# Performance work log

Measured on AMD Instinct MI355X. Metric: run time of the kernel, lower is better.

## Reference

```python
import jax, jax.numpy as jnp
import numpy as np

# Bahdanau additive attention (eval mode: dropout is identity):
#   fac1 = W @ k        [B, d, S]
#   fac2 = U @ q        [B, d, S]
#   s    = v^T tanh(fac1 + fac2)   [B, 1, S]
#   attn = softmax(s, axis=-1)

B, D, S = 32, 1024, 2048


def setup_inputs() -> dict:
    key = jax.random.key(0)
    kq, kk, kv, kW, kU = jax.random.split(key, 5)
    scale = 1.0 / np.sqrt(D)
    return {
        "q": jax.random.normal(kq, (B, D, S), dtype=jnp.float32),
        "k": jax.random.normal(kk, (B, D, S), dtype=jnp.float32),
        "v": jax.random.normal(kv, (B, D, 1), dtype=jnp.float32),
        "W": jax.random.normal(kW, (D, D), dtype=jnp.float32) * scale,
        "U": jax.random.normal(kU, (D, D), dtype=jnp.float32) * scale,
    }


def reference(q, k, v, W, U):
    # projections: [d,e] x [b,e,s] -> [b,d,s]
    fac1 = jnp.einsum("de,bes->bds", W, k)
    fac2 = jnp.einsum("de,bes->bds", U, q)
    e = jnp.tanh(fac1 + fac2)            # [B, D, S]
    s = jnp.einsum("bdo,bds->bos", v, e)  # [B, 1, S]
    attn = jax.nn.softmax(s, axis=-1)     # softmax over sequence
    return attn
```

## Files before the change

kernel.cpp:

```cpp
#include <hip/hip_runtime.h>

#define D_ 1024
#define S_ 2048
#define B_ 32
#define BM 256
#define BN 256
#define BK 64
#define NKT 32
#define NPH 64

typedef __attribute__((ext_vector_type(8))) _Float16 f16x8;
typedef __attribute__((ext_vector_type(16))) float f32x16;

__device__ __forceinline__ void async_ld16(const void* g, void* l) {
  __builtin_amdgcn_global_load_lds(
      (const __attribute__((address_space(1))) void*)g,
      (__attribute__((address_space(3))) void*)l, 16, 0, 0);
}

__global__ void prep_kernel(const float* __restrict__ W, const float* __restrict__ U,
                            _Float16* __restrict__ wf, _Float16* __restrict__ uf) {
  int t = blockIdx.x * blockDim.x + threadIdx.x;
  const float* src = blockIdx.y ? U : W;
  _Float16* dst = blockIdx.y ? uf : wf;

  int tile = t >> 11;
  int g    = t & 2047;
  int top  = g >> 6;
  int ks = top >> 3, wr = (top >> 2) & 1, fm = top & 3;
  int lane = g & 63, l31 = lane & 31, lhi = lane >> 5;
  int row   = wr * 128 + fm * 32 + l31;
  int chunk = ks * 2 + lhi;
  int d = (tile >> 4) * 256 + row;
  int e = (tile & 15) * 64 + chunk * 8;

  const float* p = src + (size_t)d * D_ + e;
  f16x8 hv;
#pragma unroll
  for (int j = 0; j < 8; ++j) hv[j] = (_Float16)p[j];
  *(f16x8*)(dst + (size_t)t * 8) = hv;
}

__global__ void kqprep_kernel(const float* __restrict__ kten, const float* __restrict__ qten,
                              _Float16* __restrict__ bfmt) {
  size_t t = (size_t)blockIdx.x * 256 + threadIdx.x;
  int g    = (int)(t & 2047);
  int tile = (int)(t >> 11);
  int st   = tile & 7;
  int ktt  = (tile >> 3) & 15;
  int half = (tile >> 7) & 1;
  int b    = tile >> 8;
  int l31 = g & 31, clh = (g >> 5) & 1, w2 = (g >> 6) & 7, cks = g >> 9;
  int n = w2 * 32 + l31;
  int c = cks * 2 + clh;
  int e = ktt * 64 + c * 8;
  int s = st * 256 + n;

  const float* src = (half ? qten : kten) + (size_t)b * (D_ * S_) + (size_t)e * S_ + s;
  f16x8 hv;
#pragma unroll
  for (int j = 0; j < 8; ++j) hv[j] = (_Float16)src[(size_t)j * S_];
  *(f16x8*)(bfmt + t * 8) = hv;
}

__global__ void __launch_bounds__(512, 2)
gemm_kernel(const float* __restrict__ v,
            const _Float16* __restrict__ wf, const _Float16* __restrict__ uf,
            const _Float16* __restrict__ bfmt,
            float* __restrict__ partials) {
  __shared__ __align__(16) _Float16 Af[4][BM * 32];
  __shared__ __align__(16) _Float16 Bf[4][BN * 32];
  __shared__ float vbuf[BM];
  __shared__ float red[2][BN];

  const int tid  = threadIdx.x;
  const int lane = tid & 63;
  const int wid  = tid >> 6;
  const int wr   = wid >> 2;
  const int wc   = wid & 3;

  int bid  = blockIdx.x;
  int g    = ((bid >> 5) << 3) | (bid & 7);
  int dblk = (bid >> 3) & 3;
  int st   = g & 7;
  int b    = g >> 3;
  int s0   = st * BN;

  if (tid < BM) vbuf[tid] = v[(size_t)b * D_ + dblk * BM + tid];
  __syncthreads();

  f32x16 acc[4][2];
#pragma unroll
  for (int i = 0; i < 4; ++i)
#pragma unroll
    for (int j = 0; j < 2; ++j)
#pragma unroll
      for (int r = 0; r < 16; ++r) acc[i][j][r] = 0.0f;

#define PH_FENCE asm volatile("" ::: "memory")
#define WAIT8 asm volatile("s_waitcnt vmcnt(8)" ::: "memory")
#define WAIT4 asm volatile("s_waitcnt vmcnt(4)" ::: "memory")
#define WAIT0 asm volatile("s_waitcnt vmcnt(0)" ::: "memory")

#define GLLH(h_) do {                                                          \
    const int kt_ = (h_) >> 1, hh_ = (h_) & 1, bi_ = (h_) & 3;                 \
    const int half_ = kt_ >> 4, ktt_ = kt_ & 15;                               \
    const _Float16* at_ = (half_ ? uf : wf)                                    \
        + (size_t)(dblk * 16 + ktt_) * 16384 + (size_t)hh_ * 8192;             \
    const _Float16* bt_ = bfmt                                                 \
        + ((size_t)(((b * 2 + half_) * 16 + ktt_) * 8 + st)) * 16384           \
        + (size_t)hh_ * 8192;                                                  \
    async_ld16(at_ + (size_t)tid * 8,         &Af[bi_][(size_t)tid * 8]);      \
    async_ld16(at_ + (size_t)(tid + 512) * 8, &Af[bi_][(size_t)(tid + 512) * 8]); \
    async_ld16(bt_ + (size_t)tid * 8,         &Bf[bi_][(size_t)tid * 8]);      \
    async_ld16(bt_ + (size_t)(tid + 512) * 8, &Bf[bi_][(size_t)(tid + 512) * 8]); \
  } while (0)

#define PHASE(h_, ISSUE, WAITC) do {                                           \
    PH_FENCE;                                                                  \
    const int bi_ = (h_) & 3;                                                  \
    f16x8 a0_[4], a1_[4], b0_[2], b1_[2];                                      \
    _Pragma("unroll")                                                          \
    for (int fm = 0; fm < 4; ++fm)                                             \
      a0_[fm] = *(const f16x8*)&Af[bi_][(size_t)(((wr * 4 + fm) * 64 + lane)) * 8]; \
    _Pragma("unroll")                                                          \
    for (int fn = 0; fn < 2; ++fn)                                             \
      b0_[fn] = *(const f16x8*)&Bf[bi_][(size_t)(((wc * 2 + fn) * 64 + lane)) * 8]; \
    _Pragma("unroll")                                                          \
    for (int fm = 0; fm < 4; ++fm)                                             \
      a1_[fm] = *(const f16x8*)&Af[bi_][(size_t)(((8 + wr * 4 + fm) * 64 + lane)) * 8]; \
    _Pragma("unroll")                                                          \
    for (int fn = 0; fn < 2; ++fn)                                             \
      b1_[fn] = *(const f16x8*)&Bf[bi_][(size_t)(((8 + wc * 2 + fn) * 64 + lane)) * 8]; \
    ISSUE;                                                                     \
    __builtin_amdgcn_s_barrier();                                              \
    __builtin_amdgcn_s_setprio(1);                                             \
    _Pragma("unroll")                                                          \
    for (int fm = 0; fm < 4; ++fm)                                             \
      _Pragma("unroll")                                                        \
      for (int fn = 0; fn < 2; ++fn)                                           \
        acc[fm][fn] = __builtin_amdgcn_mfma_f32_32x32x16_f16(a0_[fm], b0_[fn], acc[fm][fn], 0, 0, 0); \
    _Pragma("unroll")                                                          \
    for (int fm = 0; fm < 4; ++fm)                                             \
      _Pragma("unroll")                                                        \
      for (int fn = 0; fn < 2; ++fn)                                           \
        acc[fm][fn] = __builtin_amdgcn_mfma_f32_32x32x16_f16(a1_[fm], b1_[fn], acc[fm][fn], 0, 0, 0); \
    __builtin_amdgcn_s_setprio(0);                                             \
    WAITC;                                                                     \
    __builtin_amdgcn_s_barrier();                                              \
    __builtin_amdgcn_sched_barrier(0);                                         \
  } while (0)

  PH_FENCE;
  GLLH(0); GLLH(1); GLLH(2);
  WAIT8;
  __builtin_amdgcn_s_barrier();
  __builtin_amdgcn_sched_barrier(0);

  for (int h = 0; h < NPH - 3; ++h) {
    PHASE(h, GLLH(h + 3), WAIT8);
  }
  PHASE(61, , WAIT4);
  PHASE(62, , WAIT0);
  PHASE(63, , );

#undef PHASE
#undef GLLH
#undef WAIT0
#undef WAIT4
#undef WAIT8
#undef PH_FENCE

  float psum[2] = {0.f, 0.f};
#pragma unroll
  for (int fm = 0; fm < 4; ++fm)
#pragma unroll
    for (int fn = 0; fn < 2; ++fn)
#pragma unroll
      for (int r = 0; r < 16; ++r) {
        int row = wr * 128 + fm * 32 + (r & 3) + 8 * (r >> 2) + 4 * (lane >> 5);
        float x  = acc[fm][fn][r];
        float th = 1.0f - 2.0f / (__expf(2.0f * x) + 1.0f);
        psum[fn] += vbuf[row] * th;
      }
#pragma unroll
  for (int fn = 0; fn < 2; ++fn) psum[fn] += __shfl_xor(psum[fn], 32);
  if (lane < 32) {
    red[wr][wc * 64 + lane]      = psum[0];
    red[wr][wc * 64 + 32 + lane] = psum[1];
  }
  __syncthreads();
  if (tid < BN) {
    float val = red[0][tid] + red[1][tid];
    partials[(size_t)(dblk * B_ + b) * S_ + s0 + tid] = val;
  }
}

__global__ void __launch_bounds__(512, 2)
gemm_fb_kernel(const float* __restrict__ kten, const float* __restrict__ qten,
               const float* __restrict__ v,
               const _Float16* __restrict__ wf, const _Float16* __restrict__ uf,
               float* __restrict__ partials) {
  __shared__ __align__(16) _Float16 Af[2][BM * BK];
  __shared__ __align__(16) _Float16 Bf[2][BN * BK];
  __shared__ float vbuf[BM];
  __shared__ float red[2][BN];

  const int tid  = threadIdx.x;
  const int lane = tid & 63;
  const int wid  = tid >> 6;
  const int wr   = wid >> 2;
  const int wc   = wid & 3;

  int bid  = blockIdx.x;
  int g    = ((bid >> 5) << 3) | (bid & 7);
  int dblk = (bid >> 3) & 3;
  int st   = g & 7;
  int b    = g >> 3;
  int s0   = st * BN;

  if (tid < BM) vbuf[tid] = v[(size_t)b * D_ + dblk * BM + tid];

  f32x16 acc[4][2];
#pragma unroll
  for (int i = 0; i < 4; ++i)
#pragma unroll
    for (int j = 0; j < 2; ++j)
#pragma unroll
      for (int r = 0; r < 16; ++r) acc[i][j][r] = 0.0f;

  const int nB = tid & 255;
  const int kq = tid >> 8;

#define PH_FENCE_F asm volatile("" ::: "memory")
#define PH_BAR_F __builtin_amdgcn_s_barrier()

#define GLLA_F(ktn, buf, part) do {                                            \
    const int half_ = (ktn) >> 4, ktt_ = (ktn) & 15;                           \
    const _Float16* at_ = (half_ ? uf : wf) + (size_t)(dblk * 16 + ktt_) * 16384; \
    async_ld16(at_ + (size_t)(tid + (part) * 1024) * 8,                        \
               &Af[buf][(size_t)(tid + (part) * 1024) * 8]);                   \
    async_ld16(at_ + (size_t)(tid + (part) * 1024 + 512) * 8,                  \
               &Af[buf][(size_t)(tid + (part) * 1024 + 512) * 8]);             \
  } while (0)

#define LOADB_F(ktn, xv, h) do {                                               \
    const int half_ = (ktn) >> 4, ktt_ = (ktn) & 15;                           \
    const float* col_ = (half_ ? qten : kten) + (size_t)b * (D_ * S_)          \
                        + (size_t)(ktt_ * 64) * S_ + s0 + nB                   \
                        + (size_t)(kq * 32) * S_;                              \
    _Pragma("unroll")                                                          \
    for (int j = 16 * (h); j < 16 * (h) + 16; ++j) xv[j] = col_[(size_t)j * S_]; \
  } while (0)

#define CVTWRITE_F(xv, buf) do {                                               \
    _Pragma("unroll")                                                          \
    for (int cl = 0; cl < 4; ++cl) {                                           \
      f16x8 hv_;                                                               \
      _Pragma("unroll")                                                        \
      for (int w = 0; w < 8; ++w) hv_[w] = (_Float16)xv[cl * 8 + w];           \
      int c_ = kq * 4 + cl, cks_ = c_ >> 1, clh_ = c_ & 1;                     \
      int gnl_ = ((cks_ * 8 + (nB >> 6) * 2 + ((nB >> 5) & 1)) << 6)           \
                 | (clh_ << 5) | (nB & 31);                                    \
      *(f16x8*)&Bf[buf][(size_t)gnl_ * 8] = hv_;                               \
    }                                                                          \
  } while (0)

#define COMPUTE_PHASE_F(cur_, ks_) do {                                        \
    f16x8 af_[4], bf_[2];                                                      \
    _Pragma("unroll")                                                          \
    for (int fm = 0; fm < 4; ++fm)                                             \
      af_[fm] = *(const f16x8*)&Af[cur_][(size_t)(((ks_) * 8 + wr * 4 + fm) * 64 + lane) * 8]; \
    _Pragma("unroll")                                                          \
    for (int fn = 0; fn < 2; ++fn)                                             \
      bf_[fn] = *(const f16x8*)&Bf[cur_][(size_t)(((ks_) * 8 + wc * 2 + fn) * 64 + lane) * 8]; \
    __builtin_amdgcn_s_setprio(1);                                             \
    _Pragma("unroll")                                                          \
    for (int fm = 0; fm < 4; ++fm)                                             \
      _Pragma("unroll")                                                        \
      for (int fn = 0; fn < 2; ++fn)                                           \
        acc[fm][fn] = __builtin_amdgcn_mfma_f32_32x32x16_f16(af_[fm], bf_[fn], acc[fm][fn], 0, 0, 0); \
    __builtin_amdgcn_s_setprio(0);                                             \
  } while (0)

#define STEP_F(kt_, cur_, xvC_, xvN_) do {                                     \
    const int nxt_ = (cur_) ^ 1;                                               \
    PH_FENCE_F; GLLA_F((kt_) + 1, nxt_, 0); COMPUTE_PHASE_F(cur_, 0); PH_BAR_F;\
    PH_FENCE_F; GLLA_F((kt_) + 1, nxt_, 1); COMPUTE_PHASE_F(cur_, 1); PH_BAR_F;\
    PH_FENCE_F; LOADB_F((kt_) + 2, xvN_, 0); COMPUTE_PHASE_F(cur_, 2); PH_BAR_F;\
    PH_FENCE_F; LOADB_F((kt_) + 2, xvN_, 1); CVTWRITE_F(xvC_, nxt_);           \
              COMPUTE_PHASE_F(cur_, 3);                                        \
    asm volatile("s_waitcnt vmcnt(32) lgkmcnt(0)" ::: "memory");               \
    PH_BAR_F;                                                                  \
    __builtin_amdgcn_sched_barrier(0);                                         \
  } while (0)

  float xvA[32], xvB[32];
  LOADB_F(0, xvA, 0); LOADB_F(0, xvA, 1);
  GLLA_F(0, 0, 0);    GLLA_F(0, 0, 1);
  LOADB_F(1, xvB, 0); LOADB_F(1, xvB, 1);
  CVTWRITE_F(xvA, 0);
  __syncthreads();

  for (int it = 0; it < 15; ++it) {
    STEP_F(2 * it,     0, xvB, xvA);
    STEP_F(2 * it + 1, 1, xvA, xvB);
  }

  PH_FENCE_F; GLLA_F(31, 1, 0); COMPUTE_PHASE_F(0, 0); PH_BAR_F;
  PH_FENCE_F; GLLA_F(31, 1, 1); COMPUTE_PHASE_F(0, 1); PH_BAR_F;
  PH_FENCE_F; COMPUTE_PHASE_F(0, 2); PH_BAR_F;
  PH_FENCE_F; CVTWRITE_F(xvB, 1); COMPUTE_PHASE_F(0, 3);
  __syncthreads();
  COMPUTE_PHASE_F(1, 0); COMPUTE_PHASE_F(1, 1); COMPUTE_PHASE_F(1, 2); COMPUTE_PHASE_F(1, 3);

#undef STEP_F
#undef COMPUTE_PHASE_F
#undef CVTWRITE_F
#undef LOADB_F
#undef GLLA_F
#undef PH_BAR_F
#undef PH_FENCE_F

  float psum[2] = {0.f, 0.f};
#pragma unroll
  for (int fm = 0; fm < 4; ++fm)
#pragma unroll
    for (int fn = 0; fn < 2; ++fn)
#pragma unroll
      for (int r = 0; r < 16; ++r) {
        int row = wr * 128 + fm * 32 + (r & 3) + 8 * (r >> 2) + 4 * (lane >> 5);
        float x  = acc[fm][fn][r];
        float th = 1.0f - 2.0f / (__expf(2.0f * x) + 1.0f);
        psum[fn] += vbuf[row] * th;
      }
#pragma unroll
  for (int fn = 0; fn < 2; ++fn) psum[fn] += __shfl_xor(psum[fn], 32);
  if (lane < 32) {
    red[wr][wc * 64 + lane]      = psum[0];
    red[wr][wc * 64 + 32 + lane] = psum[1];
  }
  __syncthreads();
  if (tid < BN) {
    float val = red[0][tid] + red[1][tid];
    partials[(size_t)(dblk * B_ + b) * S_ + s0 + tid] = val;
  }
}

__global__ void softmax_kernel(const float* __restrict__ partials, float* __restrict__ out) {
  __shared__ float logit[S_];
  __shared__ float wred[2][4];
  int b = blockIdx.x, tid = threadIdx.x;
  int lane = tid & 63, wid = tid >> 6;
  float lmax = -1e30f;
  for (int i = tid; i < S_; i += 256) {
    float acc = 0.f;
#pragma unroll
    for (int d = 0; d < 4; ++d) acc += partials[(size_t)(d * B_ + b) * S_ + i];
    logit[i] = acc;
    lmax = fmaxf(lmax, acc);
  }
#pragma unroll
  for (int o = 32; o; o >>= 1) lmax = fmaxf(lmax, __shfl_xor(lmax, o));
  if (lane == 0) wred[0][wid] = lmax;
  __syncthreads();
  float m = fmaxf(fmaxf(wred[0][0], wred[0][1]), fmaxf(wred[0][2], wred[0][3]));
  float lsum = 0.f;
  for (int i = tid; i < S_; i += 256) {
    float ex = __expf(logit[i] - m);
    logit[i] = ex;
    lsum += ex;
  }
#pragma unroll
  for (int o = 32; o; o >>= 1) lsum += __shfl_xor(lsum, o);
  if (lane == 0) wred[1][wid] = lsum;
  __syncthreads();
  float tot = wred[1][0] + wred[1][1] + wred[1][2] + wred[1][3];
  float inv = 1.0f / tot;
  for (int i = tid; i < S_; i += 256) out[(size_t)b * S_ + i] = logit[i] * inv;
}

extern "C" void kernel_launch(void* const* d_in, const int* in_sizes, int n_in,
                              void* d_out, int out_size, void* d_ws, size_t ws_size,
                              hipStream_t stream) {
  const float* q = (const float*)d_in[0];
  const float* k = (const float*)d_in[1];
  const float* v = (const float*)d_in[2];
  const float* W = (const float*)d_in[3];
  const float* U = (const float*)d_in[4];

  _Float16* wf = (_Float16*)d_ws;
  _Float16* uf = wf + (size_t)D_ * D_;
  float* partials = (float*)(uf + (size_t)D_ * D_);
  _Float16* bfmt = (_Float16*)((char*)d_ws + 5242880);
  const size_t NEED = 5242880ull + 268435456ull;

  prep_kernel<<<dim3(512, 2), 256, 0, stream>>>(W, U, wf, uf);
  if (ws_size >= NEED) {
    kqprep_kernel<<<dim3(65536), 256, 0, stream>>>(k, q, bfmt);
    gemm_kernel<<<dim3(1024), 512, 0, stream>>>(v, wf, uf, bfmt, partials);
  } else {
    gemm_fb_kernel<<<dim3(2048 / 2), 512, 0, stream>>>(k, q, v, wf, uf, partials);
  }
  softmax_kernel<<<dim3(B_), 256, 0, stream>>>(partials, (float*)d_out);
}
```

Baseline: 418.0 us.

## Software-pipeline LDS fragment reads with MFMA using register double buffering

Restructures the GEMM main loop into half-phase sub-steps. Each sub-step issues half of a global-to-LDS async load, reads the next k-slice fragments from LDS into alternate registers, and runs MFMAs on the previously loaded fragments. The LDS read latency is meant to overlap with matrix-core work, and the global loads are spread more evenly across sub-steps. In exchange it needs more registers for the doubled fragment buffers and adds barriers per sub-step, and the vmcnt waits and buffer reuse must be ordered correctly.

```diff
diff --git a/kernel.cpp b/kernel.cpp
--- a/kernel.cpp
+++ b/kernel.cpp
@@ -7,7 +7,6 @@
 #define BN 256
 #define BK 64
 #define NKT 32
-#define NPH 64
 
 typedef __attribute__((ext_vector_type(8))) _Float16 f16x8;
 typedef __attribute__((ext_vector_type(16))) float f32x16;
@@ -99,10 +98,11 @@
 
 #define PH_FENCE asm volatile("" ::: "memory")
 #define WAIT8 asm volatile("s_waitcnt vmcnt(8)" ::: "memory")
+#define WAIT6 asm volatile("s_waitcnt vmcnt(6)" ::: "memory")
 #define WAIT4 asm volatile("s_waitcnt vmcnt(4)" ::: "memory")
 #define WAIT0 asm volatile("s_waitcnt vmcnt(0)" ::: "memory")
 
-#define GLLH(h_) do {                                                          \
+#define GLLH2(h_, part_) do {                                                  \
     const int kt_ = (h_) >> 1, hh_ = (h_) & 1, bi_ = (h_) & 3;                 \
     const int half_ = kt_ >> 4, ktt_ = kt_ & 15;                               \
     const _Float16* at_ = (half_ ? uf : wf)                                    \
@@ -110,64 +110,81 @@
     const _Float16* bt_ = bfmt                                                 \
         + ((size_t)(((b * 2 + half_) * 16 + ktt_) * 8 + st)) * 16384           \
         + (size_t)hh_ * 8192;                                                  \
-    async_ld16(at_ + (size_t)tid * 8,         &Af[bi_][(size_t)tid * 8]);      \
-    async_ld16(at_ + (size_t)(tid + 512) * 8, &Af[bi_][(size_t)(tid + 512) * 8]); \
-    async_ld16(bt_ + (size_t)tid * 8,         &Bf[bi_][(size_t)tid * 8]);      \
-    async_ld16(bt_ + (size_t)(tid + 512) * 8, &Bf[bi_][(size_t)(tid + 512) * 8]); \
-  } while (0)
-
-#define PHASE(h_, ISSUE, WAITC) do {                                           \
-    PH_FENCE;                                                                  \
-    const int bi_ = (h_) & 3;                                                  \
-    f16x8 a0_[4], a1_[4], b0_[2], b1_[2];                                      \
+    async_ld16(at_ + (size_t)(tid + (part_) * 512) * 8,                        \
+               &Af[bi_][(size_t)(tid + (part_) * 512) * 8]);                   \
+    async_ld16(bt_ + (size_t)(tid + (part_) * 512) * 8,                        \
+               &Bf[bi_][(size_t)(tid + (part_) * 512) * 8]);                   \
+  } while (0)
+
+#define DSREAD6(A_, B_, bi_, sl_) do {                                         \
     _Pragma("unroll")                                                          \
     for (int fm = 0; fm < 4; ++fm)                                             \
-      a0_[fm] = *(const f16x8*)&Af[bi_][(size_t)(((wr * 4 + fm) * 64 + lane)) * 8]; \
+      A_[fm] = *(const f16x8*)&Af[bi_][(size_t)((((sl_) * 8 + wr * 4 + fm) * 64 + lane)) * 8]; \
     _Pragma("unroll")                                                          \
     for (int fn = 0; fn < 2; ++fn)                                             \
-      b0_[fn] = *(const f16x8*)&Bf[bi_][(size_t)(((wc * 2 + fn) * 64 + lane)) * 8]; \
-    _Pragma("unroll")                                                          \
-    for (int fm = 0; fm < 4; ++fm)                                             \
-      a1_[fm] = *(const f16x8*)&Af[bi_][(size_t)(((8 + wr * 4 + fm) * 64 + lane)) * 8]; \
-    _Pragma("unroll")                                                          \
-    for (int fn = 0; fn < 2; ++fn)                                             \
-      b1_[fn] = *(const f16x8*)&Bf[bi_][(size_t)(((8 + wc * 2 + fn) * 64 + lane)) * 8]; \
-    ISSUE;                                                                     \
-    __builtin_amdgcn_s_barrier();                                              \
+      B_[fn] = *(const f16x8*)&Bf[bi_][(size_t)((((sl_) * 8 + wc * 2 + fn) * 64 + lane)) * 8]; \
+  } while (0)
+
+#define MFMA8(A_, B_) do {                                                     \
     __builtin_amdgcn_s_setprio(1);                                             \
     _Pragma("unroll")                                                          \
     for (int fm = 0; fm < 4; ++fm)                                             \
       _Pragma("unroll")                                                        \
       for (int fn = 0; fn < 2; ++fn)                                           \
-        acc[fm][fn] = __builtin_amdgcn_mfma_f32_32x32x16_f16(a0_[fm], b0_[fn], acc[fm][fn], 0, 0, 0); \
-    _Pragma("unroll")                                                          \
-    for (int fm = 0; fm < 4; ++fm)                                             \
-      _Pragma("unroll")                                                        \
-      for (int fn = 0; fn < 2; ++fn)                                           \
-        acc[fm][fn] = __builtin_amdgcn_mfma_f32_32x32x16_f16(a1_[fm], b1_[fn], acc[fm][fn], 0, 0, 0); \
+        acc[fm][fn] = __builtin_amdgcn_mfma_f32_32x32x16_f16(A_[fm], B_[fn], acc[fm][fn], 0, 0, 0); \
     __builtin_amdgcn_s_setprio(0);                                             \
+  } while (0)
+
+#define SUB(rdbi_, rdsl_, CA, CB, NA, NB, ISSUE, WAITC) do {                   \
+    PH_FENCE;                                                                  \
+    ISSUE;                                                                     \
+    DSREAD6(NA, NB, rdbi_, rdsl_);                                             \
+    __builtin_amdgcn_sched_barrier(0);                                         \
+    MFMA8(CA, CB);                                                             \
     WAITC;                                                                     \
     __builtin_amdgcn_s_barrier();                                              \
     __builtin_amdgcn_sched_barrier(0);                                         \
   } while (0)
 
+  f16x8 fa0[4], fb0[2], fa1[4], fb1[2];
+
   PH_FENCE;
-  GLLH(0); GLLH(1); GLLH(2);
+  GLLH2(0, 0); GLLH2(0, 1);
+  GLLH2(1, 0); GLLH2(1, 1);
+  GLLH2(2, 0); GLLH2(2, 1);
   WAIT8;
   __builtin_amdgcn_s_barrier();
   __builtin_amdgcn_sched_barrier(0);
-
-  for (int h = 0; h < NPH - 3; ++h) {
-    PHASE(h, GLLH(h + 3), WAIT8);
-  }
-  PHASE(61, , WAIT4);
-  PHASE(62, , WAIT0);
-  PHASE(63, , );
-
-#undef PHASE
-#undef GLLH
+  DSREAD6(fa0, fb0, 0, 0);
+
+  for (int m = 0; m < 15; ++m) {
+    const int h3 = 4 * m + 3, h4 = 4 * m + 4, h5 = 4 * m + 5, h6 = 4 * m + 6;
+    SUB(0, 1, fa0, fb0, fa1, fb1, GLLH2(h3, 0), WAIT6);
+    SUB(1, 0, fa1, fb1, fa0, fb0, GLLH2(h3, 1),      );
+    SUB(1, 1, fa0, fb0, fa1, fb1, GLLH2(h4, 0), WAIT6);
+    SUB(2, 0, fa1, fb1, fa0, fb0, GLLH2(h4, 1),      );
+    SUB(2, 1, fa0, fb0, fa1, fb1, GLLH2(h5, 0), WAIT6);
+    SUB(3, 0, fa1, fb1, fa0, fb0, GLLH2(h5, 1),      );
+    SUB(3, 1, fa0, fb0, fa1, fb1, GLLH2(h6, 0), WAIT6);
+    SUB(0, 0, fa1, fb1, fa0, fb0, GLLH2(h6, 1),      );
+  }
+  SUB(0, 1, fa0, fb0, fa1, fb1, GLLH2(63, 0), WAIT6);
+  SUB(1, 0, fa1, fb1, fa0, fb0, GLLH2(63, 1),      );
+  SUB(1, 1, fa0, fb0, fa1, fb1,             , WAIT4);
+  SUB(2, 0, fa1, fb1, fa0, fb0,             ,      );
+  SUB(2, 1, fa0, fb0, fa1, fb1,             , WAIT0);
+  SUB(3, 0, fa1, fb1, fa0, fb0,             ,      );
+  SUB(3, 1, fa0, fb0, fa1, fb1,             ,      );
+  PH_FENCE;
+  MFMA8(fa1, fb1);
+
+#undef SUB
+#undef MFMA8
+#undef DSREAD6
+#undef GLLH2
 #undef WAIT0
 #undef WAIT4
+#undef WAIT6
 #undef WAIT8
 #undef PH_FENCE
 
@@ -400,7 +417,7 @@
     kqprep_kernel<<<dim3(65536), 256, 0, stream>>>(k, q, bfmt);
     gemm_kernel<<<dim3(1024), 512, 0, stream>>>(v, wf, uf, bfmt, partials);
   } else {
-    gemm_fb_kernel<<<dim3(2048 / 2), 512, 0, stream>>>(k, q, v, wf, uf, partials);
+    gemm_fb_kernel<<<dim3(1024), 512, 0, stream>>>(k, q, v, wf, uf, partials);
   }
   softmax_kernel<<<dim3(B_), 256, 0, stream>>>(partials, (float*)d_out);
 }
```

Measured after the change: 431.8 us. 1.03x slower.

## Shrink GEMM tile to 256x128 with 4 waves and triple-buffered LDS

Applied to the files above, without the earlier changes.

The main GEMM kernel moves from 256x256 tiles with 8 waves to 256x128 tiles with 4 waves, doubling the grid to 2048 blocks. The kq prep layout is rearranged to match. The LDS ring shrinks from 4 to 3 stages, using a 3-way unrolled phase loop and an explicit lgkmcnt wait, which lowers LDS use so more blocks can be resident. The trade-off is that each wave still computes a 128x64 sub-tile, so per-block reuse of the A operand drops and A traffic from L2 per output doubles.

```diff
diff --git a/kernel.cpp b/kernel.cpp
--- a/kernel.cpp
+++ b/kernel.cpp
@@ -4,8 +4,7 @@
 #define S_ 2048
 #define B_ 32
 #define BM 256
-#define BN 256
-#define BK 64
+#define BN 128
 #define NKT 32
 #define NPH 64
 
@@ -44,17 +43,17 @@
 __global__ void kqprep_kernel(const float* __restrict__ kten, const float* __restrict__ qten,
                               _Float16* __restrict__ bfmt) {
   size_t t = (size_t)blockIdx.x * 256 + threadIdx.x;
-  int g    = (int)(t & 2047);
-  int tile = (int)(t >> 11);
-  int st   = tile & 7;
-  int ktt  = (tile >> 3) & 15;
-  int half = (tile >> 7) & 1;
-  int b    = tile >> 8;
-  int l31 = g & 31, clh = (g >> 5) & 1, w2 = (g >> 6) & 7, cks = g >> 9;
+  int g    = (int)(t & 1023);
+  int tile = (int)(t >> 10);
+  int st   = tile & 15;
+  int ktt  = (tile >> 4) & 15;
+  int half = (tile >> 8) & 1;
+  int b    = tile >> 9;
+  int l31 = g & 31, clh = (g >> 5) & 1, w2 = (g >> 6) & 3, cks = (g >> 8) & 3;
   int n = w2 * 32 + l31;
   int c = cks * 2 + clh;
   int e = ktt * 64 + c * 8;
-  int s = st * 256 + n;
+  int s = st * 128 + n;
 
   const float* src = (half ? qten : kten) + (size_t)b * (D_ * S_) + (size_t)e * S_ + s;
   f16x8 hv;
@@ -63,30 +62,30 @@
   *(f16x8*)(bfmt + t * 8) = hv;
 }
 
-__global__ void __launch_bounds__(512, 2)
+__global__ void __launch_bounds__(256, 2)
 gemm_kernel(const float* __restrict__ v,
             const _Float16* __restrict__ wf, const _Float16* __restrict__ uf,
             const _Float16* __restrict__ bfmt,
             float* __restrict__ partials) {
-  __shared__ __align__(16) _Float16 Af[4][BM * 32];
-  __shared__ __align__(16) _Float16 Bf[4][BN * 32];
+  __shared__ __align__(16) _Float16 Af[3][BM * 32];
+  __shared__ __align__(16) _Float16 Bf[3][BN * 32];
   __shared__ float vbuf[BM];
   __shared__ float red[2][BN];
 
   const int tid  = threadIdx.x;
   const int lane = tid & 63;
   const int wid  = tid >> 6;
-  const int wr   = wid >> 2;
-  const int wc   = wid & 3;
+  const int wr   = wid >> 1;
+  const int wc   = wid & 1;
 
   int bid  = blockIdx.x;
   int g    = ((bid >> 5) << 3) | (bid & 7);
   int dblk = (bid >> 3) & 3;
-  int st   = g & 7;
-  int b    = g >> 3;
+  int st   = g & 15;
+  int b    = g >> 4;
   int s0   = st * BN;
 
-  if (tid < BM) vbuf[tid] = v[(size_t)b * D_ + dblk * BM + tid];
+  vbuf[tid] = v[(size_t)b * D_ + dblk * BM + tid];
   __syncthreads();
 
   f32x16 acc[4][2];
@@ -98,42 +97,44 @@
       for (int r = 0; r < 16; ++r) acc[i][j][r] = 0.0f;
 
 #define PH_FENCE asm volatile("" ::: "memory")
-#define WAIT8 asm volatile("s_waitcnt vmcnt(8)" ::: "memory")
-#define WAIT4 asm volatile("s_waitcnt vmcnt(4)" ::: "memory")
+#define WAIT6 asm volatile("s_waitcnt vmcnt(6)" ::: "memory")
 #define WAIT0 asm volatile("s_waitcnt vmcnt(0)" ::: "memory")
 
-#define GLLH(h_) do {                                                          \
-    const int kt_ = (h_) >> 1, hh_ = (h_) & 1, bi_ = (h_) & 3;                 \
+#define GLLH(h_, bi_) do {                                                     \
+    const int kt_ = (h_) >> 1, hh_ = (h_) & 1;                                 \
     const int half_ = kt_ >> 4, ktt_ = kt_ & 15;                               \
     const _Float16* at_ = (half_ ? uf : wf)                                    \
         + (size_t)(dblk * 16 + ktt_) * 16384 + (size_t)hh_ * 8192;             \
     const _Float16* bt_ = bfmt                                                 \
-        + ((size_t)(((b * 2 + half_) * 16 + ktt_) * 8 + st)) * 16384           \
-        + (size_t)hh_ * 8192;                                                  \
-    async_ld16(at_ + (size_t)tid * 8,         &Af[bi_][(size_t)tid * 8]);      \
-    async_ld16(at_ + (size_t)(tid + 512) * 8, &Af[bi_][(size_t)(tid + 512) * 8]); \
-    async_ld16(bt_ + (size_t)tid * 8,         &Bf[bi_][(size_t)tid * 8]);      \
-    async_ld16(bt_ + (size_t)(tid + 512) * 8, &Bf[bi_][(size_t)(tid + 512) * 8]); \
-  } while (0)
-
-#define PHASE(h_, ISSUE, WAITC) do {                                           \
+        + ((size_t)(((b * 2 + half_) * 16 + ktt_) * 16 + st)) * 8192           \
+        + (size_t)hh_ * 4096;                                                  \
+    _Pragma("unroll")                                                          \
+    for (int i = 0; i < 4; ++i)                                                \
+      async_ld16(at_ + (size_t)(tid + i * 256) * 8,                            \
+                 &Af[bi_][(size_t)(tid + i * 256) * 8]);                       \
+    _Pragma("unroll")                                                          \
+    for (int i = 0; i < 2; ++i)                                                \
+      async_ld16(bt_ + (size_t)(tid + i * 256) * 8,                            \
+                 &Bf[bi_][(size_t)(tid + i * 256) * 8]);                       \
+  } while (0)
+
+#define PHASE(bi_, ISSUE, WAITC) do {                                          \
     PH_FENCE;                                                                  \
-    const int bi_ = (h_) & 3;                                                  \
     f16x8 a0_[4], a1_[4], b0_[2], b1_[2];                                      \
     _Pragma("unroll")                                                          \
-    for (int fm = 0; fm < 4; ++fm)                                             \
-      a0_[fm] = *(const f16x8*)&Af[bi_][(size_t)(((wr * 4 + fm) * 64 + lane)) * 8]; \
-    _Pragma("unroll")                                                          \
-    for (int fn = 0; fn < 2; ++fn)                                             \
-      b0_[fn] = *(const f16x8*)&Bf[bi_][(size_t)(((wc * 2 + fn) * 64 + lane)) * 8]; \
-    _Pragma("unroll")                                                          \
-    for (int fm = 0; fm < 4; ++fm)                                             \
+    for (int fm = 0; fm < 4; ++fm) {                                           \
+      a0_[fm] = *(const f16x8*)&Af[bi_][(size_t)((((wr * 4 + fm)) * 64 + lane)) * 8]; \
       a1_[fm] = *(const f16x8*)&Af[bi_][(size_t)(((8 + wr * 4 + fm) * 64 + lane)) * 8]; \
-    _Pragma("unroll")                                                          \
-    for (int fn = 0; fn < 2; ++fn)                                             \
-      b1_[fn] = *(const f16x8*)&Bf[bi_][(size_t)(((8 + wc * 2 + fn) * 64 + lane)) * 8]; \
+    }                                                                          \
+    _Pragma("unroll")                                                          \
+    for (int fn = 0; fn < 2; ++fn) {                                           \
+      b0_[fn] = *(const f16x8*)&Bf[bi_][(size_t)((((wc * 2 + fn)) * 64 + lane)) * 8]; \
+      b1_[fn] = *(const f16x8*)&Bf[bi_][(size_t)(((4 + wc * 2 + fn) * 64 + lane)) * 8]; \
+    }                                                                          \
     ISSUE;                                                                     \
     __builtin_amdgcn_s_barrier();                                              \
+    asm volatile("s_waitcnt lgkmcnt(0)" ::: "memory");                         \
+    __builtin_amdgcn_sched_barrier(0);                                         \
     __builtin_amdgcn_s_setprio(1);                                             \
     _Pragma("unroll")                                                          \
     for (int fm = 0; fm < 4; ++fm)                                             \
@@ -152,23 +153,27 @@
   } while (0)
 
   PH_FENCE;
-  GLLH(0); GLLH(1); GLLH(2);
-  WAIT8;
+  GLLH(0, 0);
+  GLLH(1, 1);
+  WAIT6;
   __builtin_amdgcn_s_barrier();
   __builtin_amdgcn_sched_barrier(0);
 
-  for (int h = 0; h < NPH - 3; ++h) {
-    PHASE(h, GLLH(h + 3), WAIT8);
-  }
-  PHASE(61, , WAIT4);
-  PHASE(62, , WAIT0);
-  PHASE(63, , );
+  for (int m = 0; m < 20; ++m) {
+    const int h = 3 * m;
+    PHASE(0, GLLH(h + 2, 2), WAIT6);
+    PHASE(1, GLLH(h + 3, 0), WAIT6);
+    PHASE(2, GLLH(h + 4, 1), WAIT6);
+  }
+  PHASE(0, GLLH(62, 2), WAIT6);
+  PHASE(1, GLLH(63, 0), WAIT6);
+  PHASE(2, , WAIT0);
+  PHASE(0, , );
 
 #undef PHASE
 #undef GLLH
 #undef WAIT0
-#undef WAIT4
-#undef WAIT8
+#undef WAIT6
 #undef PH_FENCE
 
   float psum[2] = {0.f, 0.f};
@@ -201,10 +206,10 @@
                const float* __restrict__ v,
                const _Float16* __restrict__ wf, const _Float16* __restrict__ uf,
                float* __restrict__ partials) {
-  __shared__ __align__(16) _Float16 Af[2][BM * BK];
-  __shared__ __align__(16) _Float16 Bf[2][BN * BK];
-  __shared__ float vbuf[BM];
-  __shared__ float red[2][BN];
+  __shared__ __align__(16) _Float16 Af[2][256 * 64];
+  __shared__ __align__(16) _Float16 Bf[2][256 * 64];
+  __shared__ float vbuf[256];
+  __shared__ float red[2][256];
 
   const int tid  = threadIdx.x;
   const int lane = tid & 63;
@@ -217,9 +222,9 @@
   int dblk = (bid >> 3) & 3;
   int st   = g & 7;
   int b    = g >> 3;
-  int s0   = st * BN;
-
-  if (tid < BM) vbuf[tid] = v[(size_t)b * D_ + dblk * BM + tid];
+  int s0   = st * 256;
+
+  if (tid < 256) vbuf[tid] = v[(size_t)b * D_ + dblk * 256 + tid];
 
   f32x16 acc[4][2];
 #pragma unroll
@@ -341,7 +346,7 @@
     red[wr][wc * 64 + 32 + lane] = psum[1];
   }
   __syncthreads();
-  if (tid < BN) {
+  if (tid < 256) {
     float val = red[0][tid] + red[1][tid];
     partials[(size_t)(dblk * B_ + b) * S_ + s0 + tid] = val;
   }
@@ -398,9 +403,9 @@
   prep_kernel<<<dim3(512, 2), 256, 0, stream>>>(W, U, wf, uf);
   if (ws_size >= NEED) {
     kqprep_kernel<<<dim3(65536), 256, 0, stream>>>(k, q, bfmt);
-    gemm_kernel<<<dim3(1024), 512, 0, stream>>>(v, wf, uf, bfmt, partials);
+    gemm_kernel<<<dim3(2048), 256, 0, stream>>>(v, wf, uf, bfmt, partials);
   } else {
-    gemm_fb_kernel<<<dim3(2048 / 2), 512, 0, stream>>>(k, q, v, wf, uf, partials);
+    gemm_fb_kernel<<<dim3(1024), 512, 0, stream>>>(k, q, v, wf, uf, partials);
   }
   softmax_kernel<<<dim3(B_), 256, 0, stream>>>(partials, (float*)d_out);
 }
```

Measured after the change: 426.9 us. 2.1% more time.
